# Performance work log

Hardware: AMD Instinct MI355X
Metric: run time of the kernel (lower is better)

The kernel has to match this reference:

```python
import jax, jax.numpy as jnp
import numpy as np

N, S, D, DOUT, ATTEN, NUM_ATTR = 10000, 20, 512, 512, 64, 9

def setup_inputs() -> dict:
    key = jax.random.key(0)
    ks = jax.random.split(key, 9)
    return {
        "self_vecs": jax.random.normal(ks[0], (N, D), dtype=jnp.float32),
        "neigh_vecs": jax.random.normal(ks[1], (N, S, D), dtype=jnp.float32),
        "neigh_weight": jax.random.uniform(ks[2], (N, S, 1), dtype=jnp.float32),
        "neigh_column": jax.random.randint(ks[3], (N, S, 1), 0, NUM_ATTR, dtype=jnp.int32),
        "neigh_weights": jax.random.normal(ks[4], (D, DOUT), dtype=jnp.float32) * (1.0 / np.sqrt(D)),
        "self_weights": jax.random.normal(ks[5], (D, DOUT), dtype=jnp.float32) * (1.0 / np.sqrt(D)),
        "alpha": jax.random.normal(ks[6], (NUM_ATTR,), dtype=jnp.float32),
        "self_atten": jax.random.normal(ks[7], (D, ATTEN), dtype=jnp.float32) * (1.0 / np.sqrt(D)),
        "neigh_atten": jax.random.normal(ks[8], (D, ATTEN), dtype=jnp.float32) * (1.0 / np.sqrt(D)),
        "v": jax.random.normal(jax.random.fold_in(key, 99), (ATTEN, 1), dtype=jnp.float32) * (1.0 / np.sqrt(ATTEN)),
    }

def reference(self_vecs, neigh_vecs, neigh_weight, neigh_column,
              neigh_weights, self_weights, alpha, self_atten, neigh_atten, v):
    # per-neighbor edge weighting
    nv = neigh_vecs * neigh_weight                      # [N,S,D]
    # gather alpha by attribute column, softmax over neighbors (axis=1)
    a = alpha[neigh_column[..., 0]][..., None]          # [N,S,1]
    a_exp = jnp.exp(a)
    atten = a_exp / jnp.sum(a_exp, axis=1, keepdims=True)
    nv = nv * atten
    # dropout = 0.0 -> identity
    neigh_sum = jnp.sum(nv, axis=1)                     # [N,D]
    from_neighs = neigh_sum @ neigh_weights             # [N,DOUT]
    from_self = self_vecs @ self_weights                # [N,DOUT]
    self_ai = self_vecs @ self_atten                    # [N,ATTEN]
    neigh_ai = neigh_sum @ neigh_atten                  # [N,ATTEN]
    imp_self = self_ai + self_ai
    imp_neigh = neigh_ai + self_ai
    a_self = jnp.exp(jnp.tanh(imp_self @ v))            # [N,1]
    a_neigh = jnp.exp(jnp.tanh(imp_neigh @ v))          # [N,1]
    denom = a_self + a_neigh
    out = (a_self / denom) * from_self + (a_neigh / denom) * from_neighs
    return jax.nn.relu(out)
```

## Files before the change

kernel.cpp:

```cpp
#include <hip/hip_runtime.h>
#include <hip/hip_bf16.h>

#define N_NODES 10000
#define S_NB 20
#define D_IN 512
#define D_OUT 512
#define ATTEN_D 64
#define KTOT 1024
#define M_PAD 10048

typedef __bf16 bf16_t;
typedef bf16_t bf16x8 __attribute__((ext_vector_type(8)));
typedef float f32x4 __attribute__((ext_vector_type(4)));
typedef unsigned short u16x8 __attribute__((ext_vector_type(8)));

__device__ __forceinline__ unsigned short f2bf(float f) {
    unsigned int u = __float_as_uint(f);
    unsigned int r = u + 0x7FFFu + ((u >> 16) & 1u);
    return (unsigned short)(r >> 16);
}

__device__ __forceinline__ void gl_lds16(const unsigned short* g, unsigned short* l) {
    __builtin_amdgcn_global_load_lds(
        (const __attribute__((address_space(1))) void*)g,
        (__attribute__((address_space(3))) void*)l,
        16, 0, 0);
}

__global__ void prep_kernel(const float* __restrict__ neigh_w,
                            const float* __restrict__ self_w,
                            const float* __restrict__ self_atten,
                            const float* __restrict__ neigh_atten,
                            const float* __restrict__ v,
                            float* __restrict__ u_self, float* __restrict__ u_neigh,
                            unsigned short* __restrict__ Wt,
                            unsigned short* __restrict__ X) {
    int idx = blockIdx.x * blockDim.x + threadIdx.x;
    int stride = gridDim.x * blockDim.x;

    for (int i = idx; i < D_OUT * KTOT; i += stride) {
        int n = i >> 10;
        int k = i & (KTOT - 1);
        float w = (k < D_IN) ? self_w[k * D_OUT + n] : neigh_w[(k - D_IN) * D_OUT + n];
        Wt[i] = f2bf(w);
    }
    for (int i = idx; i < 2 * D_IN; i += stride) {
        const float* row = (i < D_IN) ? (self_atten + (size_t)i * ATTEN_D)
                                      : (neigh_atten + (size_t)(i - D_IN) * ATTEN_D);
        float s = 0.f;
        #pragma unroll
        for (int j = 0; j < ATTEN_D; ++j) s = fmaf(row[j], v[j], s);
        if (i < D_IN) u_self[i] = s; else u_neigh[i - D_IN] = s;
    }
    for (int i = idx; i < (M_PAD - N_NODES) * KTOT; i += stride) {
        X[(size_t)N_NODES * KTOT + i] = 0;
    }
}

__global__ __launch_bounds__(256) void aggregate_kernel(
        const float* __restrict__ self_vecs, const float* __restrict__ neigh_vecs,
        const float* __restrict__ neigh_weight, const int* __restrict__ neigh_column,
        const float* __restrict__ alpha,
        const float* __restrict__ u_self, const float* __restrict__ u_neigh,
        unsigned short* __restrict__ X) {
    const int lane = threadIdx.x & 63;
    const int n = blockIdx.x * 4 + (threadIdx.x >> 6);

    float e = 0.f, wgt = 0.f;
    if (lane < S_NB) {
        e = expf(alpha[neigh_column[n * S_NB + lane]]);
        wgt = neigh_weight[n * S_NB + lane];
    }
    float ssum = e;
    #pragma unroll
    for (int off = 32; off > 0; off >>= 1) ssum += __shfl_xor(ssum, off, 64);
    float coefv = wgt * e / ssum;

    const float4* nb = (const float4*)(neigh_vecs + (size_t)n * S_NB * D_IN);
    float4 acc0 = make_float4(0.f, 0.f, 0.f, 0.f);
    float4 acc1 = make_float4(0.f, 0.f, 0.f, 0.f);
    #pragma unroll
    for (int s = 0; s < S_NB; ++s) {
        float c = __shfl(coefv, s, 64);
        float4 x0 = nb[s * 128 + 2 * lane];
        float4 x1 = nb[s * 128 + 2 * lane + 1];
        acc0.x = fmaf(c, x0.x, acc0.x); acc0.y = fmaf(c, x0.y, acc0.y);
        acc0.z = fmaf(c, x0.z, acc0.z); acc0.w = fmaf(c, x0.w, acc0.w);
        acc1.x = fmaf(c, x1.x, acc1.x); acc1.y = fmaf(c, x1.y, acc1.y);
        acc1.z = fmaf(c, x1.z, acc1.z); acc1.w = fmaf(c, x1.w, acc1.w);
    }

    const float4* svp = (const float4*)(self_vecs + (size_t)n * D_IN);
    float4 sv0 = svp[2 * lane], sv1 = svp[2 * lane + 1];
    float4 us0 = ((const float4*)u_self)[2 * lane];
    float4 us1 = ((const float4*)u_self)[2 * lane + 1];
    float4 un0 = ((const float4*)u_neigh)[2 * lane];
    float4 un1 = ((const float4*)u_neigh)[2 * lane + 1];
    float p1 = sv0.x * us0.x + sv0.y * us0.y + sv0.z * us0.z + sv0.w * us0.w
             + sv1.x * us1.x + sv1.y * us1.y + sv1.z * us1.z + sv1.w * us1.w;
    float p2 = acc0.x * un0.x + acc0.y * un0.y + acc0.z * un0.z + acc0.w * un0.w
             + acc1.x * un1.x + acc1.y * un1.y + acc1.z * un1.z + acc1.w * un1.w;
    #pragma unroll
    for (int off = 32; off > 0; off >>= 1) {
        p1 += __shfl_xor(p1, off, 64);
        p2 += __shfl_xor(p2, off, 64);
    }
    float a_s = expf(tanhf(2.0f * p1));
    float a_n = expf(tanhf(p2 + p1));
    float inv = 1.0f / (a_s + a_n);
    float gs = a_s * inv, gn = a_n * inv;

    unsigned short* xrow = X + (size_t)n * KTOT;
    u16x8 o;
    o[0] = f2bf(gs * sv0.x); o[1] = f2bf(gs * sv0.y);
    o[2] = f2bf(gs * sv0.z); o[3] = f2bf(gs * sv0.w);
    o[4] = f2bf(gs * sv1.x); o[5] = f2bf(gs * sv1.y);
    o[6] = f2bf(gs * sv1.z); o[7] = f2bf(gs * sv1.w);
    *(u16x8*)(xrow + 8 * lane) = o;
    o[0] = f2bf(gn * acc0.x); o[1] = f2bf(gn * acc0.y);
    o[2] = f2bf(gn * acc0.z); o[3] = f2bf(gn * acc0.w);
    o[4] = f2bf(gn * acc1.x); o[5] = f2bf(gn * acc1.y);
    o[6] = f2bf(gn * acc1.z); o[7] = f2bf(gn * acc1.w);
    *(u16x8*)(xrow + D_IN + 8 * lane) = o;
}

#define BM 64
#define BN 128
#define BK 64

__global__ __launch_bounds__(256) void gemm_kernel(
        const unsigned short* __restrict__ X, const unsigned short* __restrict__ Wt,
        float* __restrict__ out) {
    __shared__ __align__(16) unsigned short As[BM * BK];
    __shared__ __align__(16) unsigned short Bs[BN * BK];
    const int tid = threadIdx.x;
    const int lane = tid & 63;
    const int wid = tid >> 6;
    const int m0 = blockIdx.y * BM;
    const int n0 = blockIdx.x * BN;
    const int wm = (wid >> 1) * 32;
    const int wn = (wid & 1) * 64;
    const int quad = lane >> 4;
    const int mrow = lane & 15;

    f32x4 acc[2][4];
    f32x4 zero = {0.f, 0.f, 0.f, 0.f};
    #pragma unroll
    for (int i = 0; i < 2; ++i)
        #pragma unroll
        for (int j = 0; j < 4; ++j) acc[i][j] = zero;

    const int srow = tid >> 3;
    const int skp  = (tid & 7) * 8;
    const unsigned short* gA0 = X  + (size_t)(m0 + srow) * KTOT + skp;
    const unsigned short* gA1 = X  + (size_t)(m0 + 32 + srow) * KTOT + skp;
    const unsigned short* gB0 = Wt + (size_t)(n0 + srow) * KTOT + skp;
    const unsigned short* gB1 = Wt + (size_t)(n0 + 32 + srow) * KTOT + skp;
    const unsigned short* gB2 = Wt + (size_t)(n0 + 64 + srow) * KTOT + skp;
    const unsigned short* gB3 = Wt + (size_t)(n0 + 96 + srow) * KTOT + skp;
    unsigned short* lA0 = As + tid * 8;
    unsigned short* lA1 = As + 2048 + tid * 8;
    unsigned short* lB0 = Bs + tid * 8;
    unsigned short* lB1 = Bs + 2048 + tid * 8;
    unsigned short* lB2 = Bs + 4096 + tid * 8;
    unsigned short* lB3 = Bs + 6144 + tid * 8;

    for (int k0 = 0; k0 < KTOT; k0 += BK) {
        __syncthreads();
        gl_lds16(gA0 + k0, lA0);
        gl_lds16(gA1 + k0, lA1);
        gl_lds16(gB0 + k0, lB0);
        gl_lds16(gB1 + k0, lB1);
        gl_lds16(gB2 + k0, lB2);
        gl_lds16(gB3 + k0, lB3);
        __syncthreads();

        #pragma unroll
        for (int s = 0; s < 2; ++s) {
            bf16x8 a[2], b[4];
            #pragma unroll
            for (int i = 0; i < 2; ++i)
                a[i] = *(const bf16x8*)(As + (wm + i * 16 + mrow) * BK + s * 32 + quad * 8);
            #pragma unroll
            for (int j = 0; j < 4; ++j)
                b[j] = *(const bf16x8*)(Bs + (wn + j * 16 + mrow) * BK + s * 32 + quad * 8);
            #pragma unroll
            for (int i = 0; i < 2; ++i)
                #pragma unroll
                for (int j = 0; j < 4; ++j)
                    acc[i][j] = __builtin_amdgcn_mfma_f32_16x16x32_bf16(a[i], b[j], acc[i][j], 0, 0, 0);
        }
    }

    #pragma unroll
    for (int i = 0; i < 2; ++i) {
        int rbase = m0 + wm + i * 16 + quad * 4;
        #pragma unroll
        for (int j = 0; j < 4; ++j) {
            int c = n0 + wn + j * 16 + mrow;
            #pragma unroll
            for (int r = 0; r < 4; ++r) {
                int R = rbase + r;
                if (R < N_NODES)
                    out[(size_t)R * D_OUT + c] = fmaxf(acc[i][j][r], 0.f);
            }
        }
    }
}

extern "C" void kernel_launch(void* const* d_in, const int* in_sizes, int n_in,
                              void* d_out, int out_size, void* d_ws, size_t ws_size,
                              hipStream_t stream) {
    const float* self_vecs     = (const float*)d_in[0];
    const float* neigh_vecs    = (const float*)d_in[1];
    const float* neigh_weight  = (const float*)d_in[2];
    const int*   neigh_column  = (const int*)d_in[3];
    const float* neigh_weights = (const float*)d_in[4];
    const float* self_weights  = (const float*)d_in[5];
    const float* alpha         = (const float*)d_in[6];
    const float* self_atten    = (const float*)d_in[7];
    const float* neigh_atten   = (const float*)d_in[8];
    const float* v             = (const float*)d_in[9];
    float* out = (float*)d_out;

    char* ws = (char*)d_ws;
    float* u_self  = (float*)ws;
    float* u_neigh = u_self + D_IN;
    unsigned short* Wt = (unsigned short*)(ws + 4096);
    unsigned short* X  = (unsigned short*)(ws + 4096 + (size_t)D_OUT * KTOT * 2);

    hipLaunchKernelGGL(prep_kernel, dim3(1024), dim3(256), 0, stream,
                       neigh_weights, self_weights, self_atten, neigh_atten, v,
                       u_self, u_neigh, Wt, X);
    hipLaunchKernelGGL(aggregate_kernel, dim3(N_NODES / 4), dim3(256), 0, stream,
                       self_vecs, neigh_vecs, neigh_weight, neigh_column, alpha,
                       u_self, u_neigh, X);
    hipLaunchKernelGGL(gemm_kernel, dim3(D_OUT / BN, M_PAD / BM), dim3(256), 0, stream,
                       X, Wt, out);
}
```

Baseline: 594.2 us.

## Tile weight transpose via LDS, drop X padding zeroing, reverse aggregate order

The weight transpose in prep is rewritten as a 64x64 LDS-tiled transpose so that both global reads and writes are coalesced, and the launch shrinks to 128 blocks. The zero-fill of X's padding rows is removed; instead the GEMM clamps A row indices to the last valid row, so padded rows only feed outputs that are never stored. Aggregate now processes nodes in reverse order, presumably so the last-written X rows are still in cache when the GEMM starts, and it hoists the self-vector loads ahead of the neighbor loop. These changes aim to cut prep cost and improve cache reuse between kernels, at the cost of padded GEMM rows computing on duplicated data.

```diff
diff --git a/kernel.cpp b/kernel.cpp
--- a/kernel.cpp
+++ b/kernel.cpp
@@ -27,24 +27,39 @@
         16, 0, 0);
 }
 
-__global__ void prep_kernel(const float* __restrict__ neigh_w,
-                            const float* __restrict__ self_w,
-                            const float* __restrict__ self_atten,
-                            const float* __restrict__ neigh_atten,
-                            const float* __restrict__ v,
-                            float* __restrict__ u_self, float* __restrict__ u_neigh,
-                            unsigned short* __restrict__ Wt,
-                            unsigned short* __restrict__ X) {
-    int idx = blockIdx.x * blockDim.x + threadIdx.x;
-    int stride = gridDim.x * blockDim.x;
-
-    for (int i = idx; i < D_OUT * KTOT; i += stride) {
-        int n = i >> 10;
-        int k = i & (KTOT - 1);
-        float w = (k < D_IN) ? self_w[k * D_OUT + n] : neigh_w[(k - D_IN) * D_OUT + n];
-        Wt[i] = f2bf(w);
-    }
-    for (int i = idx; i < 2 * D_IN; i += stride) {
+__global__ __launch_bounds__(256) void prep_kernel(
+        const float* __restrict__ neigh_w,
+        const float* __restrict__ self_w,
+        const float* __restrict__ self_atten,
+        const float* __restrict__ neigh_atten,
+        const float* __restrict__ v,
+        float* __restrict__ u_self, float* __restrict__ u_neigh,
+        unsigned short* __restrict__ Wt) {
+    __shared__ float tile[64][65];
+    const int tid = threadIdx.x;
+    const int half = blockIdx.x >> 6;
+    const int rem  = blockIdx.x & 63;
+    const int n0 = (rem & 7) * 64;
+    const int k0 = (rem >> 3) * 64;
+    const float* src = half ? neigh_w : self_w;
+
+    #pragma unroll
+    for (int it = 0; it < 16; ++it) {
+        int idx = it * 256 + tid;
+        int r = idx >> 6, c = idx & 63;
+        tile[r][c] = src[(size_t)(k0 + r) * D_OUT + n0 + c];
+    }
+    __syncthreads();
+    #pragma unroll
+    for (int it = 0; it < 16; ++it) {
+        int idx = it * 256 + tid;
+        int r2 = idx >> 6, c2 = idx & 63;
+        Wt[(size_t)(n0 + r2) * KTOT + half * D_IN + k0 + c2] = f2bf(tile[c2][r2]);
+    }
+
+    int gi = blockIdx.x * 8 + (tid >> 5);
+    int i = blockIdx.x * 256 + tid;
+    if (i < 2 * D_IN) {
         const float* row = (i < D_IN) ? (self_atten + (size_t)i * ATTEN_D)
                                       : (neigh_atten + (size_t)(i - D_IN) * ATTEN_D);
         float s = 0.f;
@@ -52,9 +67,7 @@
         for (int j = 0; j < ATTEN_D; ++j) s = fmaf(row[j], v[j], s);
         if (i < D_IN) u_self[i] = s; else u_neigh[i - D_IN] = s;
     }
-    for (int i = idx; i < (M_PAD - N_NODES) * KTOT; i += stride) {
-        X[(size_t)N_NODES * KTOT + i] = 0;
-    }
+    (void)gi;
 }
 
 __global__ __launch_bounds__(256) void aggregate_kernel(
@@ -64,7 +77,14 @@
         const float* __restrict__ u_self, const float* __restrict__ u_neigh,
         unsigned short* __restrict__ X) {
     const int lane = threadIdx.x & 63;
-    const int n = blockIdx.x * 4 + (threadIdx.x >> 6);
+    const int n = (N_NODES - 1) - (blockIdx.x * 4 + (threadIdx.x >> 6));
+
+    const float4* svp = (const float4*)(self_vecs + (size_t)n * D_IN);
+    float4 sv0 = svp[2 * lane], sv1 = svp[2 * lane + 1];
+    float4 us0 = ((const float4*)u_self)[2 * lane];
+    float4 us1 = ((const float4*)u_self)[2 * lane + 1];
+    float4 un0 = ((const float4*)u_neigh)[2 * lane];
+    float4 un1 = ((const float4*)u_neigh)[2 * lane + 1];
 
     float e = 0.f, wgt = 0.f;
     if (lane < S_NB) {
@@ -90,12 +110,6 @@
         acc1.z = fmaf(c, x1.z, acc1.z); acc1.w = fmaf(c, x1.w, acc1.w);
     }
 
-    const float4* svp = (const float4*)(self_vecs + (size_t)n * D_IN);
-    float4 sv0 = svp[2 * lane], sv1 = svp[2 * lane + 1];
-    float4 us0 = ((const float4*)u_self)[2 * lane];
-    float4 us1 = ((const float4*)u_self)[2 * lane + 1];
-    float4 un0 = ((const float4*)u_neigh)[2 * lane];
-    float4 un1 = ((const float4*)u_neigh)[2 * lane + 1];
     float p1 = sv0.x * us0.x + sv0.y * us0.y + sv0.z * us0.z + sv0.w * us0.w
              + sv1.x * us1.x + sv1.y * us1.y + sv1.z * us1.z + sv1.w * us1.w;
     float p2 = acc0.x * un0.x + acc0.y * un0.y + acc0.z * un0.z + acc0.w * un0.w
@@ -152,8 +166,10 @@
 
     const int srow = tid >> 3;
     const int skp  = (tid & 7) * 8;
-    const unsigned short* gA0 = X  + (size_t)(m0 + srow) * KTOT + skp;
-    const unsigned short* gA1 = X  + (size_t)(m0 + 32 + srow) * KTOT + skp;
+    const int ra0 = min(m0 + srow, N_NODES - 1);
+    const int ra1 = min(m0 + 32 + srow, N_NODES - 1);
+    const unsigned short* gA0 = X  + (size_t)ra0 * KTOT + skp;
+    const unsigned short* gA1 = X  + (size_t)ra1 * KTOT + skp;
     const unsigned short* gB0 = Wt + (size_t)(n0 + srow) * KTOT + skp;
     const unsigned short* gB1 = Wt + (size_t)(n0 + 32 + srow) * KTOT + skp;
     const unsigned short* gB2 = Wt + (size_t)(n0 + 64 + srow) * KTOT + skp;
@@ -229,9 +245,9 @@
     unsigned short* Wt = (unsigned short*)(ws + 4096);
     unsigned short* X  = (unsigned short*)(ws + 4096 + (size_t)D_OUT * KTOT * 2);
 
-    hipLaunchKernelGGL(prep_kernel, dim3(1024), dim3(256), 0, stream,
+    hipLaunchKernelGGL(prep_kernel, dim3(128), dim3(256), 0, stream,
                        neigh_weights, self_weights, self_atten, neigh_atten, v,
-                       u_self, u_neigh, Wt, X);
+                       u_self, u_neigh, Wt);
     hipLaunchKernelGGL(aggregate_kernel, dim3(N_NODES / 4), dim3(256), 0, stream,
                        self_vecs, neigh_vecs, neigh_weight, neigh_column, alpha,
                        u_self, u_neigh, X);
```

Result: no change. 601.0 us (+1.2%).
